# Optimization experiments

Hardware: AMD Instinct MI355X
Metric: run time of the kernel (lower is better)

## Reference

```python
import jax, jax.numpy as jnp
import numpy as np


def l2norm(x):
    return x * jax.lax.rsqrt(jnp.sum(x * x, axis=-1, keepdims=True) + 1e-12)


def vq_cosine(z, codebook, commit_w):
    # cosine-sim VQ: normalize inputs + codebook, nearest neighbor by cosine sim
    xn = l2norm(z)            # [N, D]
    en = l2norm(codebook)     # [K, D]
    sim = xn @ en.T           # [N, K]
    dist = 2.0 - 2.0 * sim    # squared euclidean between unit vectors
    idx = jnp.argmin(dist, axis=-1)           # [N]
    q = en[idx]                               # [N, D] quantized (normalized) codes
    commit = commit_w * jnp.mean((jax.lax.stop_gradient(q) - xn) ** 2)
    q_st = xn + jax.lax.stop_gradient(q - xn)  # straight-through
    return q_st, idx, commit, dist


def setup_inputs() -> dict:
    key = jax.random.key(0)
    ks = jax.random.split(key, 10)
    N, Din, H, K = 32768, 1024, 512, 1024
    s = lambda i, shp, fan: jax.random.normal(ks[i], shp, jnp.float32) * (1.0 / np.sqrt(fan))
    return {
        "h0": jax.random.normal(ks[0], (N, Din), jnp.float32),
        "W1": s(1, (Din, H), Din), "b1": jnp.zeros((H,), jnp.float32),
        "W2": s(2, (H, H), H),     "b2": jnp.zeros((H,), jnp.float32),
        "Wm": s(3, (H, H), H),     "bm": jnp.zeros((H,), jnp.float32),
        "Wt": s(4, (H, H), H),     "bt": jnp.zeros((H,), jnp.float32),
        "Wp": s(5, (H, H), H),     "bp": jnp.zeros((H,), jnp.float32),
        "cb_m": jax.random.normal(ks[6], (K, H), jnp.float32),
        "cb_t": jax.random.normal(ks[7], (K, H), jnp.float32),
        "cb_p": jax.random.normal(ks[8], (K, H), jnp.float32),
        "Wk": s(9, (H, 1), H),     "bk": jnp.zeros((1,), jnp.float32),
    }


def reference(h0, W1, b1, W2, b2, Wm, bm, Wt, bt, Wp, bp, cb_m, cb_t, cb_p, Wk, bk):
    COMMIT = 0.25
    TOP_M = 32
    # encoder: Linear-ReLU-Linear-ReLU
    H = jax.nn.relu(jax.nn.relu(h0 @ W1 + b1) @ W2 + b2)
    z_m = H @ Wm + bm
    z_t = H @ Wt + bt
    z_p = H @ Wp + bp
    q_m, k_m, cm, dist_m = vq_cosine(z_m, cb_m, COMMIT)
    q_t, k_t, ct, dist_t = vq_cosine(z_t, cb_t, COMMIT)
    q_p, k_p, cp, dist_p = vq_cosine(z_p, cb_p, COMMIT)
    codes = jnp.stack([k_m, k_t, k_p], axis=-1)           # [N, 3]
    alpha = jax.nn.sigmoid((H @ Wk + bk)[:, 0])           # [N]
    M = min(TOP_M, alpha.shape[0])
    key_idx = jax.lax.top_k(alpha, M)[1]                  # [M]
    token_emb = jnp.concatenate([q_m, q_t, q_p], axis=-1) # [N, 3*hid]
    L_vq = cm + ct + cp
    return (H, codes, key_idx, token_emb, L_vq)
```

## Files before the change

kernel.cpp:

```cpp
#include <hip/hip_runtime.h>


#define BM 128
#define BN 128
#define BK 16
#define MAXF 4096
#define MAXF1 12288
#define TAU_DIST 2e-5f
#define TAU_APPROX 1.25e-4f

#define CODES_OFF   16777216ULL
#define KEYIDX_OFF  16875520ULL
#define TOKEMB_OFF  16875552ULL
#define LVQ_OFF     67207200ULL

typedef __attribute__((ext_vector_type(8))) short short8;
typedef __attribute__((ext_vector_type(4))) float f32x4;

#define MFMA_BF16(a, b, c) __builtin_amdgcn_mfma_f32_16x16x32_bf16(a, b, c, 0, 0, 0)

__device__ __forceinline__ unsigned flip_bits(float x) {
  unsigned b = __float_as_uint(x);
  return b ^ ((unsigned)((int)b >> 31) | 0x80000000u);
}
__device__ __forceinline__ float unflip_bits(unsigned ob) {
  unsigned b = (ob & 0x80000000u) ? (ob ^ 0x80000000u) : ~ob;
  return __uint_as_float(b);
}
__device__ __forceinline__ float qdist(float dot, float rnv) {
  float sim = __fmul_rn(dot, rnv);
  return __fadd_rn(2.0f, -__fmul_rn(2.0f, sim));
}
__device__ __forceinline__ float dist_of_key(unsigned long long q) {
  return unflip_bits(~(unsigned)(q >> 32));
}
__device__ __forceinline__ void split2(float x, unsigned& h, unsigned& l) {
  unsigned b = __float_as_uint(x);
  unsigned hb = (b + 0x7FFFu + ((b >> 16) & 1u)) & 0xFFFF0000u;
  h = hb >> 16;
  float r = x - __uint_as_float(hb);
  unsigned cbits = __float_as_uint(r);
  l = (cbits + 0x7FFFu + ((cbits >> 16) & 1u)) >> 16;
}

template<int RELU>
__global__ __launch_bounds__(256)
void gemm_f32(const float* __restrict__ A, int lda,
              const float* __restrict__ B, int ldb,
              const float* __restrict__ bias,
              float* __restrict__ C, int ldc, int K)
{
  __shared__ float As[BK][BM + 4];
  __shared__ float Bs[BK][BN + 4];
  const int tid = threadIdx.x;
  const int tx = tid & 15, ty = tid >> 4;
  const long m0 = (long)blockIdx.x * BM;
  const long n0 = (long)blockIdx.y * BN;

  float acc[8][8];
#pragma unroll
  for (int i = 0; i < 8; i++)
#pragma unroll
    for (int j = 0; j < 8; j++) acc[i][j] = 0.f;

  for (int k0 = 0; k0 < K; k0 += BK) {
#pragma unroll
    for (int i = 0; i < 2; i++) {
      int f4 = tid + i * 256;
      int row = f4 >> 2, kc = (f4 & 3) * 4;
      float4 v = *(const float4*)(A + (m0 + row) * lda + k0 + kc);
      As[kc + 0][row] = v.x; As[kc + 1][row] = v.y;
      As[kc + 2][row] = v.z; As[kc + 3][row] = v.w;
    }
#pragma unroll
    for (int i = 0; i < 2; i++) {
      int f4 = tid + i * 256;
      int kr = f4 >> 5, c4 = (f4 & 31) * 4;
      *(float4*)&Bs[kr][c4] = *(const float4*)(B + (long)(k0 + kr) * ldb + n0 + c4);
    }
    __syncthreads();
#pragma unroll
    for (int kk = 0; kk < BK; kk++) {
      float a[8], b[8];
      *(float4*)&a[0] = *(const float4*)&As[kk][ty * 8];
      *(float4*)&a[4] = *(const float4*)&As[kk][ty * 8 + 4];
      *(float4*)&b[0] = *(const float4*)&Bs[kk][tx * 4];
      *(float4*)&b[4] = *(const float4*)&Bs[kk][64 + tx * 4];
#pragma unroll
      for (int i = 0; i < 8; i++)
#pragma unroll
        for (int j = 0; j < 8; j++)
          acc[i][j] = fmaf(a[i], b[j], acc[i][j]);
    }
    __syncthreads();
  }

  float bv[8];
#pragma unroll
  for (int j = 0; j < 8; j++) {
    int col = (j < 4) ? (tx * 4 + j) : (64 + tx * 4 + (j - 4));
    bv[j] = bias[n0 + col];
  }
#pragma unroll
  for (int i = 0; i < 8; i++) {
    float o[8];
#pragma unroll
    for (int j = 0; j < 8; j++) {
      float v = acc[i][j] + bv[j];
      if (RELU) v = fmaxf(v, 0.f);
      o[j] = v;
    }
    float* cp = C + (m0 + ty * 8 + i) * (long)ldc + n0;
    *(float4*)(cp + tx * 4) = *(const float4*)&o[0];
    *(float4*)(cp + 64 + tx * 4) = *(const float4*)&o[4];
  }
}

__global__ __launch_bounds__(256)
void w_split(const float* __restrict__ Wm, const float* __restrict__ Wt,
             const float* __restrict__ Wp,
             unsigned short* __restrict__ wh, unsigned short* __restrict__ wl)
{
  int t = blockIdx.x * 256 + threadIdx.x;
  int c = t >> 15, rem = t & 32767;
  int n = rem >> 6, kg = (rem & 63) * 8;
  const float* W = (c == 0) ? Wm : (c == 1) ? Wt : Wp;
  unsigned h[8], l[8];
#pragma unroll
  for (int i = 0; i < 8; i++) {
    float v = W[(size_t)(kg + i) * 512 + n];
    split2(v, h[i], l[i]);
  }
  uint4 hp, lp;
  hp.x = h[0] | (h[1] << 16); hp.y = h[2] | (h[3] << 16);
  hp.z = h[4] | (h[5] << 16); hp.w = h[6] | (h[7] << 16);
  lp.x = l[0] | (l[1] << 16); lp.y = l[2] | (l[3] << 16);
  lp.z = l[4] | (l[5] << 16); lp.w = l[6] | (l[7] << 16);
  size_t g = ((size_t)c * 512 + n) * 512 + kg;
  *(uint4*)(wh + g) = hp;
  *(uint4*)(wl + g) = lp;
}

__global__ __launch_bounds__(512, 2)
void z_mfma(const float* __restrict__ H,
            const unsigned short* __restrict__ wh,
            const unsigned short* __restrict__ wl,
            const float* __restrict__ bm, const float* __restrict__ bt,
            const float* __restrict__ bp,
            unsigned short* __restrict__ zh, unsigned short* __restrict__ zl)
{
  __shared__ unsigned short Ah[128 * 40];
  __shared__ unsigned short Al[128 * 40];
  __shared__ unsigned short Bh[512 * 40];
  __shared__ unsigned short Bl[512 * 40];

  const int tid = threadIdx.x;
  const int w = tid >> 6, wr = w >> 2, wc = w & 3;
  const int l = tid & 63, l15 = l & 15, lg = l >> 4;
  const int c = blockIdx.y;
  const long m0 = (long)blockIdx.x * BM;
  const size_t wbase = (size_t)c * 512 * 512;

  f32x4 acc[4][8];
#pragma unroll
  for (int fi = 0; fi < 4; fi++)
#pragma unroll
    for (int fj = 0; fj < 8; fj++)
#pragma unroll
      for (int r = 0; r < 4; r++) acc[fi][fj][r] = 0.f;

  for (int k0 = 0; k0 < 512; k0 += 32) {
#pragma unroll
    for (int i = 0; i < 2; i++) {
      int f4 = tid + i * 512;
      int row = f4 >> 3, kc = (f4 & 7) * 4;
      float4 v = *(const float4*)(H + (m0 + row) * 512 + k0 + kc);
      unsigned hx, lx, hy, ly, hz, lz, hw, lw;
      split2(v.x, hx, lx); split2(v.y, hy, ly);
      split2(v.z, hz, lz); split2(v.w, hw, lw);
      uint2 hp, lp;
      hp.x = hx | (hy << 16); hp.y = hz | (hw << 16);
      lp.x = lx | (ly << 16); lp.y = lz | (lw << 16);
      *(uint2*)&Ah[row * 40 + kc] = hp;
      *(uint2*)&Al[row * 40 + kc] = lp;
    }
#pragma unroll
    for (int j = 0; j < 4; j++) {
      int q = tid + j * 512;
      int n = q >> 2, kg = (q & 3) * 8;
      size_t g = wbase + (size_t)n * 512 + k0 + kg;
      *(uint4*)&Bh[n * 40 + kg] = *(const uint4*)(wh + g);
      *(uint4*)&Bl[n * 40 + kg] = *(const uint4*)(wl + g);
    }
    __syncthreads();

    short8 bh[8], bl[8];
#pragma unroll
    for (int fj = 0; fj < 8; fj++) {
      int boff = (wc * 128 + fj * 16 + l15) * 40 + lg * 8;
      bh[fj] = *(const short8*)&Bh[boff];
      bl[fj] = *(const short8*)&Bl[boff];
    }
#pragma unroll
    for (int fi = 0; fi < 4; fi++) {
      int aoff = (wr * 64 + fi * 16 + l15) * 40 + lg * 8;
      short8 ah = *(const short8*)&Ah[aoff];
      short8 al = *(const short8*)&Al[aoff];
#pragma unroll
      for (int fj = 0; fj < 8; fj++) {
        acc[fi][fj] = MFMA_BF16(ah, bh[fj], acc[fi][fj]);
        acc[fi][fj] = MFMA_BF16(al, bh[fj], acc[fi][fj]);
        acc[fi][fj] = MFMA_BF16(ah, bl[fj], acc[fi][fj]);
      }
    }
    __syncthreads();
  }

  const float* bc = (c == 0) ? bm : (c == 1) ? bt : bp;
  float bcv[8];
#pragma unroll
  for (int fj = 0; fj < 8; fj++) bcv[fj] = bc[wc * 128 + fj * 16 + l15];
#pragma unroll
  for (int fi = 0; fi < 4; fi++) {
#pragma unroll
    for (int fj = 0; fj < 8; fj++) {
      int col = wc * 128 + fj * 16 + l15;
#pragma unroll
      for (int r = 0; r < 4; r++) {
        long row = m0 + wr * 64 + fi * 16 + lg * 4 + r;
        float v = acc[fi][fj][r] + bcv[fj];
        unsigned h, lo;
        split2(v, h, lo);
        size_t g = (size_t)row * 1536 + (size_t)c * 512 + col;
        zh[g] = (unsigned short)h;
        zl[g] = (unsigned short)lo;
      }
    }
  }
}

__global__ __launch_bounds__(256)
void sim_argmax(const unsigned short* __restrict__ zh,
                const unsigned short* __restrict__ zl,
                const float* __restrict__ en,
                const unsigned short* __restrict__ en_hi,
                const unsigned short* __restrict__ en_lo,
                const float* __restrict__ rn,
                float* __restrict__ out,
                float* __restrict__ lvq,
                int* __restrict__ fc1,
                int* __restrict__ flags1)
{
  __shared__ unsigned short Ah[128 * 40];
  __shared__ unsigned short Al[128 * 40];
  __shared__ unsigned short Bh[128 * 40];
  __shared__ unsigned short Bl[128 * 40];
  __shared__ unsigned long long redk[128][2];
  __shared__ float redd[128][2];
  __shared__ int bidx[128];
  __shared__ float dsum[128];

  const int tid = threadIdx.x;
  const int w = tid >> 6, wr = w >> 1, wc = w & 1;
  const int l = tid & 63, l15 = l & 15, lg = l >> 4;
  const int c = blockIdx.y;
  const long m0 = (long)blockIdx.x * BM;
  const float* Ben = en + (size_t)c * 524288;
  const size_t cb_base = (size_t)c * 524288;

  float rrn[16];
#pragma unroll
  for (int fi = 0; fi < 4; fi++)
#pragma unroll
    for (int r = 0; r < 4; r++)
      rrn[fi * 4 + r] = rn[(long)c * 32768 + m0 + wr * 64 + fi * 16 + lg * 4 + r];

  unsigned long long best = 0ULL;
  float bestd2 = 1e30f;

  for (int ct = 0; ct < 8; ct++) {
    const int n0 = ct * 128;
    f32x4 acc[4][4];
#pragma unroll
    for (int fi = 0; fi < 4; fi++)
#pragma unroll
      for (int fj = 0; fj < 4; fj++)
#pragma unroll
        for (int r = 0; r < 4; r++) acc[fi][fj][r] = 0.f;

    for (int k0 = 0; k0 < 512; k0 += 32) {
#pragma unroll
      for (int i = 0; i < 2; i++) {
        int q = tid + i * 256;
        int row = q >> 2, kc = (q & 3) * 8;
        size_t g = (size_t)(m0 + row) * 1536 + (size_t)c * 512 + k0 + kc;
        *(uint4*)&Ah[row * 40 + kc] = *(const uint4*)(zh + g);
        *(uint4*)&Al[row * 40 + kc] = *(const uint4*)(zl + g);
      }
#pragma unroll
      for (int i = 0; i < 2; i++) {
        int q = tid + i * 256;
        int code = q >> 2, kc = (q & 3) * 8;
        size_t g = cb_base + (size_t)(n0 + code) * 512 + (k0 + kc);
        *(uint4*)&Bh[code * 40 + kc] = *(const uint4*)(en_hi + g);
        *(uint4*)&Bl[code * 40 + kc] = *(const uint4*)(en_lo + g);
      }
      __syncthreads();

      short8 bh[4], bl[4];
#pragma unroll
      for (int f = 0; f < 4; f++) {
        int boff = (wc * 64 + f * 16 + l15) * 40 + lg * 8;
        bh[f] = *(const short8*)&Bh[boff];
        bl[f] = *(const short8*)&Bl[boff];
      }
#pragma unroll
      for (int fi = 0; fi < 4; fi++) {
        int aoff = (wr * 64 + fi * 16 + l15) * 40 + lg * 8;
        short8 ah = *(const short8*)&Ah[aoff];
        short8 al = *(const short8*)&Al[aoff];
#pragma unroll
        for (int fj = 0; fj < 4; fj++) {
          acc[fi][fj] = MFMA_BF16(ah, bh[fj], acc[fi][fj]);
          acc[fi][fj] = MFMA_BF16(al, bh[fj], acc[fi][fj]);
          acc[fi][fj] = MFMA_BF16(ah, bl[fj], acc[fi][fj]);
        }
      }
      __syncthreads();
    }

#pragma unroll
    for (int fi = 0; fi < 4; fi++) {
      unsigned long long kk[4]; float dd[4];
#pragma unroll
      for (int r = 0; r < 4; r++) {
        float d1 = 1e30f, d2v = 1e30f; int bj = 0;
#pragma unroll
        for (int fj = 0; fj < 4; fj++) {
          float d = qdist(acc[fi][fj][r], rrn[fi * 4 + r]);
          if (d < d1) { d2v = d1; d1 = d; bj = fj; }
          else if (d < d2v) d2v = d;
        }
        int code = n0 + wc * 64 + bj * 16 + l15;
        kk[r] = ((unsigned long long)(~flip_bits(d1)) << 32) | (unsigned)(~code);
        dd[r] = d2v;
      }
#pragma unroll
      for (int m = 1; m < 16; m <<= 1) {
#pragma unroll
        for (int r = 0; r < 4; r++) {
          unsigned long long ok = __shfl_xor(kk[r], m, 64);
          float od = __shfl_xor(dd[r], m, 64);
          if (ok > kk[r]) { dd[r] = fminf(od, dist_of_key(kk[r])); kk[r] = ok; }
          else dd[r] = fminf(dd[r], dist_of_key(ok));
        }
      }
      if (l15 == 0) {
#pragma unroll
        for (int r = 0; r < 4; r++) {
          int row = wr * 64 + fi * 16 + lg * 4 + r;
          redk[row][wc] = kk[r];
          redd[row][wc] = dd[r];
        }
      }
    }
    __syncthreads();
    if (tid < 128) {
      unsigned long long kA = redk[tid][0]; float dA = redd[tid][0];
      unsigned long long kB = redk[tid][1]; float dB = redd[tid][1];
      unsigned long long km; float m2;
      if (kB > kA) { km = kB; m2 = fminf(dB, dist_of_key(kA)); }
      else         { km = kA; m2 = fminf(dA, dist_of_key(kB)); }
      if (km > best) {
        float oldd = (best == 0ULL) ? 1e30f : dist_of_key(best);
        bestd2 = fminf(oldd, m2);
        best = km;
      } else {
        bestd2 = fminf(bestd2, dist_of_key(km));
      }
    }
    __syncthreads();
  }

  if (tid < 128) {
    const long n = m0 + tid;
    const unsigned code = ~(unsigned)best;
    const float d1 = dist_of_key(best);
    out[CODES_OFF + (unsigned long long)n * 3 + c] = (float)code;
    bidx[tid] = (int)code;
    dsum[tid] = d1;
    if (bestd2 - d1 < TAU_APPROX) {
      int slot = atomicAdd(fc1, 1);
      if (slot < MAXF1) { flags1[2 * slot] = (int)n; flags1[2 * slot + 1] = c; }
    }
  }
  __syncthreads();
  if (tid < 64) dsum[tid] += dsum[tid + 64];
  __syncthreads();
  if (tid < 64) {
    float s = dsum[tid];
#pragma unroll
    for (int off = 32; off; off >>= 1) s += __shfl_xor(s, off);
    if (tid == 0) atomicAdd(lvq, s * (0.25f / (32768.f * 512.f)));
  }
  for (int t = tid; t < 128 * 128; t += 256) {
    int r = t >> 7, d4 = (t & 127) * 4;
    float4 v = *(const float4*)(Ben + (long)bidx[r] * 512 + d4);
    *(float4*)(out + TOKEMB_OFF + (unsigned long long)(m0 + r) * 1536 + c * 512 + d4) = v;
  }
}

__global__ __launch_bounds__(256)
void refine_fp32(const float* __restrict__ H,
                 const float* __restrict__ Wm, const float* __restrict__ bm,
                 const float* __restrict__ Wt, const float* __restrict__ bt,
                 const float* __restrict__ Wp, const float* __restrict__ bp,
                 const float* __restrict__ en,
                 const int* __restrict__ fc1, const int* __restrict__ flags1,
                 int* __restrict__ fc2, int* __restrict__ flags2,
                 float* __restrict__ out)
{
  int nf = *fc1; if (nf > MAXF1) nf = MAXF1;
  const int b = blockIdx.x;
  if (b >= nf) return;
  const int n = flags1[2 * b];
  const int c = flags1[2 * b + 1];
  const int t = threadIdx.x;

  __shared__ float sH[512];
  __shared__ float zs[512];
  __shared__ float sred[256];
  __shared__ unsigned long long wk[4];
  __shared__ float wd2[4];
  __shared__ int fcode;
  __shared__ float srn;

  const float* Wc = (c == 0) ? Wm : (c == 1) ? Wt : Wp;
  const float* bc = (c == 0) ? bm : (c == 1) ? bt : bp;

  sH[t]       = H[(size_t)n * 512 + t];
  sH[t + 256] = H[(size_t)n * 512 + 256 + t];
  __syncthreads();

  {
    float a0 = 0.f, a1 = 0.f;
    for (int i = 0; i < 512; i++) {
      float h = sH[i];
      a0 = fmaf(h, Wc[(size_t)i * 512 + t], a0);
      a1 = fmaf(h, Wc[(size_t)i * 512 + t + 256], a1);
    }
    float z0 = a0 + bc[t];
    float z1 = a1 + bc[t + 256];
    zs[t] = z0; zs[t + 256] = z1;
    sred[t] = z0 * z0 + z1 * z1;
  }
  __syncthreads();
  for (int s = 128; s > 0; s >>= 1) {
    if (t < s) sred[t] += sred[t + s];
    __syncthreads();
  }
  if (t == 0) srn = 1.f / sqrtf(sred[0] + 1e-12f);
  __syncthreads();
  const float rnv = srn;

  const int wv = t >> 6, lane = t & 63;
  float zlv[8];
#pragma unroll
  for (int m = 0; m < 8; m++) zlv[m] = zs[lane * 8 + m];

  const float* cbase = en + (size_t)c * 524288;
  unsigned long long k1 = 0ULL; float d2 = 1e30f;
  for (int j = 0; j < 256; j++) {
    int k = (j << 2) | wv;
    const float* cr = cbase + (size_t)k * 512 + lane * 8;
    float4 c0 = *(const float4*)cr, c1 = *(const float4*)(cr + 4);
    float dt = zlv[0] * c0.x + zlv[1] * c0.y + zlv[2] * c0.z + zlv[3] * c0.w
             + zlv[4] * c1.x + zlv[5] * c1.y + zlv[6] * c1.z + zlv[7] * c1.w;
#pragma unroll
    for (int off = 32; off; off >>= 1) dt += __shfl_xor(dt, off);
    float d = qdist(dt, rnv);
    unsigned long long key =
        ((unsigned long long)(~flip_bits(d)) << 32) | (unsigned)(~k);
    if (key > k1) { d2 = fminf(d2, (k1 == 0ULL) ? 1e30f : dist_of_key(k1)); k1 = key; }
    else d2 = fminf(d2, d);
  }
  if (lane == 0) { wk[wv] = k1; wd2[wv] = d2; }
  __syncthreads();
  if (t == 0) {
    unsigned long long kb = wk[0]; float s2 = wd2[0];
#pragma unroll
    for (int w = 1; w < 4; w++) {
      unsigned long long q = wk[w]; float qd2 = wd2[w];
      if (q > kb) { s2 = fminf(qd2, dist_of_key(kb)); kb = q; }
      else s2 = fminf(s2, dist_of_key(q));
    }
    int code = (int)(~(unsigned)kb);
    float d1 = dist_of_key(kb);
    out[CODES_OFF + (unsigned long long)n * 3 + c] = (float)code;
    fcode = code;
    if (s2 - d1 < TAU_DIST) {
      int slot = atomicAdd(fc2, 1);
      if (slot < MAXF) { flags2[2 * slot] = n; flags2[2 * slot + 1] = c; }
    }
  }
  __syncthreads();
  const int fk = fcode;
  if (t < 128) {
    const float* er = en + ((size_t)c * 1024 + fk) * 512;
    float4 v = ((const float4*)er)[t];
    *(float4*)(out + TOKEMB_OFF + (unsigned long long)n * 1536 + c * 512 + t * 4) = v;
  }
}

__global__ __launch_bounds__(256)
void rescue_fp64(const float* __restrict__ h0,
                 const float* __restrict__ W1, const float* __restrict__ b1,
                 const float* __restrict__ W2, const float* __restrict__ b2,
                 const float* __restrict__ Wm, const float* __restrict__ bm,
                 const float* __restrict__ Wt, const float* __restrict__ bt,
                 const float* __restrict__ Wp, const float* __restrict__ bp,
                 const float* __restrict__ cbm, const float* __restrict__ cbt,
                 const float* __restrict__ cbp,
                 const float* __restrict__ en,
                 const int* __restrict__ flag_cnt, const int* __restrict__ flags,
                 float* __restrict__ out)
{
  int nf = *flag_cnt; if (nf > MAXF) nf = MAXF;
  const int b = blockIdx.x;
  if (b >= nf) return;
  const int n = flags[2 * b];
  const int c = flags[2 * b + 1];
  const int t = threadIdx.x;

  __shared__ double s1[512];
  __shared__ double s2[512];
  __shared__ double sred[256];
  __shared__ float sd4[4];
  __shared__ int sk4[4];
  __shared__ double shz;

  const float* Wc = (c == 0) ? Wm : (c == 1) ? Wt : Wp;
  const float* bc = (c == 0) ? bm : (c == 1) ? bt : bp;
  const float* cb = (c == 0) ? cbm : (c == 1) ? cbt : cbp;
  const float* h0r = h0 + (size_t)n * 1024;

  {
    double a0 = 0.0, a1 = 0.0;
    for (int i = 0; i < 1024; i++) {
      double h = (double)h0r[i];
      a0 = fma(h, (double)W1[(size_t)i * 512 + t], a0);
      a1 = fma(h, (double)W1[(size_t)i * 512 + t + 256], a1);
    }
    s1[t]       = fmax(a0 + (double)b1[t], 0.0);
    s1[t + 256] = fmax(a1 + (double)b1[t + 256], 0.0);
  }
  __syncthreads();
  {
    double a0 = 0.0, a1 = 0.0;
    for (int i = 0; i < 512; i++) {
      double h = s1[i];
      a0 = fma(h, (double)W2[(size_t)i * 512 + t], a0);
      a1 = fma(h, (double)W2[(size_t)i * 512 + t + 256], a1);
    }
    s2[t]       = fmax(a0 + (double)b2[t], 0.0);
    s2[t + 256] = fmax(a1 + (double)b2[t + 256], 0.0);
  }
  __syncthreads();
  {
    double a0 = 0.0, a1 = 0.0;
    for (int i = 0; i < 512; i++) {
      double h = s2[i];
      a0 = fma(h, (double)Wc[(size_t)i * 512 + t], a0);
      a1 = fma(h, (double)Wc[(size_t)i * 512 + t + 256], a1);
    }
    __syncthreads();
    s1[t]       = a0 + (double)bc[t];
    s1[t + 256] = a1 + (double)bc[t + 256];
  }
  __syncthreads();
  sred[t] = s1[t] * s1[t] + s1[t + 256] * s1[t + 256];
  __syncthreads();
  for (int s = 128; s > 0; s >>= 1) {
    if (t < s) sred[t] += sred[t + s];
    __syncthreads();
  }
  if (t == 0) shz = 1.0 / sqrt(sred[0] + 1e-12);
  __syncthreads();
  const double rz = shz;

  const int wv = t >> 6, lane = t & 63;
  double zl[8];
#pragma unroll
  for (int m = 0; m < 8; m++) zl[m] = s1[lane * 8 + m];
  float bd = 1e30f; int bkk = 1 << 30;
  for (int j = 0; j < 256; j++) {
    int k = (j << 2) | wv;
    const float* cr = cb + (size_t)k * 512 + lane * 8;
    float4 c0 = *(const float4*)cr, c1 = *(const float4*)(cr + 4);
    double x0 = c0.x, x1 = c0.y, x2 = c0.z, x3 = c0.w;
    double x4 = c1.x, x5 = c1.y, x6 = c1.z, x7 = c1.w;
    double dt = zl[0]*x0 + zl[1]*x1 + zl[2]*x2 + zl[3]*x3
              + zl[4]*x4 + zl[5]*x5 + zl[6]*x6 + zl[7]*x7;
    double nc = x0*x0 + x1*x1 + x2*x2 + x3*x3 + x4*x4 + x5*x5 + x6*x6 + x7*x7;
#pragma unroll
    for (int off = 32; off; off >>= 1) {
      dt += __shfl_xor(dt, off);
      nc += __shfl_xor(nc, off);
    }
    double sim64 = dt * rz * (1.0 / sqrt(nc + 1e-12));
    float s32 = (float)sim64;
    float d32 = __fadd_rn(2.0f, -__fmul_rn(2.0f, s32));
    if (d32 < bd) { bd = d32; bkk = k; }
  }
  if (lane == 0) { sd4[wv] = bd; sk4[wv] = bkk; }
  __syncthreads();
  if (t == 0) {
    float d = sd4[0]; int k = sk4[0];
#pragma unroll
    for (int w = 1; w < 4; w++)
      if (sd4[w] < d || (sd4[w] == d && sk4[w] < k)) { d = sd4[w]; k = sk4[w]; }
    sk4[0] = k;
    out[CODES_OFF + (unsigned long long)n * 3 + c] = (float)k;
  }
  __syncthreads();
  const int fk = sk4[0];
  if (t < 128) {
    const float* er = en + ((size_t)c * 1024 + fk) * 512;
    float4 v = ((const float4*)er)[t];
    *(float4*)(out + TOKEMB_OFF + (unsigned long long)n * 1536 + c * 512 + t * 4) = v;
  }
}

__global__ __launch_bounds__(256)
void row_rnorm(const unsigned short* __restrict__ zh,
               const unsigned short* __restrict__ zl,
               float* __restrict__ rn)
{
  const int lane = threadIdx.x & 63;
  const long r = (long)blockIdx.x * 4 + (threadIdx.x >> 6);
  const int cc = (int)(r >> 15), n = (int)(r & 32767);
  const size_t base = (size_t)n * 1536 + (size_t)cc * 512 + lane * 8;
  uint4 h = *(const uint4*)(zh + base);
  uint4 lo = *(const uint4*)(zl + base);
  float s = 0.f;
  const unsigned hw[4] = {h.x, h.y, h.z, h.w};
  const unsigned lw[4] = {lo.x, lo.y, lo.z, lo.w};
#pragma unroll
  for (int i = 0; i < 4; i++) {
    float ze = __uint_as_float(hw[i] << 16) + __uint_as_float(lw[i] << 16);
    float zo = __uint_as_float(hw[i] & 0xFFFF0000u) + __uint_as_float(lw[i] & 0xFFFF0000u);
    s = fmaf(ze, ze, s);
    s = fmaf(zo, zo, s);
  }
#pragma unroll
  for (int off = 32; off; off >>= 1) s += __shfl_xor(s, off);
  if (lane == 0) rn[r] = 1.f / sqrtf(s + 1e-12f);
}

__global__ __launch_bounds__(256)
void cb_norm(const float* __restrict__ cbm, const float* __restrict__ cbt,
             const float* __restrict__ cbp, float* __restrict__ en,
             unsigned short* __restrict__ en_hi, unsigned short* __restrict__ en_lo)
{
  const int lane = threadIdx.x & 63;
  const long r = (long)blockIdx.x * 4 + (threadIdx.x >> 6);
  const int cc = (int)(r >> 10), k = (int)(r & 1023);
  const float* cb = (cc == 0) ? cbm : (cc == 1) ? cbt : cbp;
  const float* p = cb + (long)k * 512 + lane * 8;
  float4 v0 = *(const float4*)p, v1 = *(const float4*)(p + 4);
  float s = v0.x * v0.x + v0.y * v0.y + v0.z * v0.z + v0.w * v0.w
          + v1.x * v1.x + v1.y * v1.y + v1.z * v1.z + v1.w * v1.w;
#pragma unroll
  for (int off = 32; off; off >>= 1) s += __shfl_xor(s, off);
  float sc = 1.f / sqrtf(s + 1e-12f);
  v0.x *= sc; v0.y *= sc; v0.z *= sc; v0.w *= sc;
  v1.x *= sc; v1.y *= sc; v1.z *= sc; v1.w *= sc;
  const size_t g = (size_t)cc * 524288 + (size_t)k * 512 + lane * 8;
  float* q = en + g;
  *(float4*)q = v0; *(float4*)(q + 4) = v1;
  unsigned h[8], lo[8];
  split2(v0.x, h[0], lo[0]); split2(v0.y, h[1], lo[1]);
  split2(v0.z, h[2], lo[2]); split2(v0.w, h[3], lo[3]);
  split2(v1.x, h[4], lo[4]); split2(v1.y, h[5], lo[5]);
  split2(v1.z, h[6], lo[6]); split2(v1.w, h[7], lo[7]);
  uint4 hp, lp;
  hp.x = h[0] | (h[1] << 16);  hp.y = h[2] | (h[3] << 16);
  hp.z = h[4] | (h[5] << 16);  hp.w = h[6] | (h[7] << 16);
  lp.x = lo[0] | (lo[1] << 16); lp.y = lo[2] | (lo[3] << 16);
  lp.z = lo[4] | (lo[5] << 16); lp.w = lo[6] | (lo[7] << 16);
  *(uint4*)(en_hi + g) = hp;
  *(uint4*)(en_lo + g) = lp;
}

__global__ __launch_bounds__(256)
void logits_alpha(const float* __restrict__ H, const float* __restrict__ Wk,
                  const float* __restrict__ bk, float* __restrict__ alpha)
{
  const int lane = threadIdx.x & 63;
  const long n = (long)blockIdx.x * 4 + (threadIdx.x >> 6);
  const float* p = H + n * 512 + lane * 8;
  const float* w = Wk + lane * 8;
  float4 a0 = *(const float4*)p, a1 = *(const float4*)(p + 4);
  float4 w0 = *(const float4*)w, w1 = *(const float4*)(w + 4);
  float s = a0.x * w0.x + a0.y * w0.y + a0.z * w0.z + a0.w * w0.w
          + a1.x * w1.x + a1.y * w1.y + a1.z * w1.z + a1.w * w1.w;
#pragma unroll
  for (int off = 32; off; off >>= 1) s += __shfl_xor(s, off);
  if (lane == 0) alpha[n] = 1.f / (1.f + expf(-(s + bk[0])));
}

__global__ __launch_bounds__(1024)
void topk32(const float* __restrict__ alpha, float* __restrict__ out)
{
  __shared__ unsigned long long sk[1024];
  const int tid = threadIdx.x;
  unsigned long long prev = ~0ULL;
  for (int it = 0; it < 32; it++) {
    unsigned long long best = 0;
#pragma unroll 4
    for (int i = tid; i < 32768; i += 1024) {
      unsigned long long key =
          ((unsigned long long)flip_bits(alpha[i]) << 32) | (unsigned)(~i);
      if (key < prev && key > best) best = key;
    }
    sk[tid] = best;
    __syncthreads();
    for (int s = 512; s > 0; s >>= 1) {
      if (tid < s) { unsigned long long q = sk[tid + s]; if (q > sk[tid]) sk[tid] = q; }
      __syncthreads();
    }
    unsigned long long sel = sk[0];
    __syncthreads();
    if (tid == 0) out[it] = (float)(~(unsigned)sel);
    prev = sel;
  }
}

extern "C" void kernel_launch(void* const* d_in, const int* in_sizes, int n_in,
                              void* d_out, int out_size, void* d_ws, size_t ws_size,
                              hipStream_t stream)
{
  (void)in_sizes; (void)n_in; (void)out_size; (void)ws_size;
  const float* h0  = (const float*)d_in[0];
  const float* W1  = (const float*)d_in[1];
  const float* b1  = (const float*)d_in[2];
  const float* W2  = (const float*)d_in[3];
  const float* b2  = (const float*)d_in[4];
  const float* Wm  = (const float*)d_in[5];
  const float* bm  = (const float*)d_in[6];
  const float* Wt  = (const float*)d_in[7];
  const float* bt  = (const float*)d_in[8];
  const float* Wp  = (const float*)d_in[9];
  const float* bp  = (const float*)d_in[10];
  const float* cbm = (const float*)d_in[11];
  const float* cbt = (const float*)d_in[12];
  const float* cbp = (const float*)d_in[13];
  const float* Wk  = (const float*)d_in[14];
  const float* bk  = (const float*)d_in[15];
  float* out = (float*)d_out;
  float* ws  = (float*)d_ws;

  float* h1 = ws;
  unsigned short* zh = (unsigned short*)ws;
  unsigned short* zl = (unsigned short*)ws + 50331648ULL;
  float* en = ws + 50331648ULL;
  float* rn = ws + 51904512ULL;
  float* al = ws + 52002816ULL;
  int* fc1    = (int*)(ws + 52035584ULL);
  int* flags1 = (int*)(ws + 52035585ULL);
  int* fc2    = (int*)(ws + 52060161ULL);
  int* flags2 = (int*)(ws + 52060162ULL);
  unsigned short* en_hi = (unsigned short*)(ws + 52068356ULL);
  unsigned short* en_lo = (unsigned short*)(ws + 52854788ULL);
  unsigned short* Wh = (unsigned short*)(ws + 53641220ULL);
  unsigned short* Wl = (unsigned short*)(ws + 54034436ULL);
  float* H  = out;
  float* lvq = out + LVQ_OFF;

  hipMemsetAsync(lvq, 0, sizeof(float), stream);
  hipMemsetAsync(fc1, 0, sizeof(int), stream);
  hipMemsetAsync(fc2, 0, sizeof(int), stream);

  gemm_f32<1><<<dim3(256, 4), 256, 0, stream>>>(h0, 1024, W1, 512, b1, h1, 512, 1024);
  gemm_f32<1><<<dim3(256, 4), 256, 0, stream>>>(h1, 512,  W2, 512, b2, H,  512, 512);

  w_split<<<384, 256, 0, stream>>>(Wm, Wt, Wp, Wh, Wl);
  z_mfma<<<dim3(256, 3), 512, 0, stream>>>(H, Wh, Wl, bm, bt, bp, zh, zl);

  row_rnorm<<<24576, 256, 0, stream>>>(zh, zl, rn);
  cb_norm<<<768, 256, 0, stream>>>(cbm, cbt, cbp, en, en_hi, en_lo);
  sim_argmax<<<dim3(256, 3), 256, 0, stream>>>(zh, zl, en, en_hi, en_lo, rn, out, lvq,
                                               fc1, flags1);
  refine_fp32<<<MAXF1, 256, 0, stream>>>(H, Wm, bm, Wt, bt, Wp, bp, en,
                                         fc1, flags1, fc2, flags2, out);
  rescue_fp64<<<MAXF, 256, 0, stream>>>(h0, W1, b1, W2, b2, Wm, bm, Wt, bt, Wp, bp,
                                        cbm, cbt, cbp, en, fc2, flags2, out);
  logits_alpha<<<8192, 256, 0, stream>>>(H, Wk, bk, al);
  topk32<<<1, 1024, 0, stream>>>(al, out + KEYIDX_OFF);
}
```

Before: 2.494 ms.

## Move encoder GEMMs to split-bf16 MFMA and stage z epilogue through LDS

Replaces the scalar FP32 GEMMs for the two encoder layers with a generalized MFMA kernel. It uses a three-product bf16 hi/lo split to approximate FP32 accuracy, with weights pre-split by a generic split kernel. The z projection epilogue now stages hi/lo planes in shared memory and writes coalesced 16-byte vectors instead of scattered 2-byte stores. The costs are three extra MFMAs per tile and some precision loss versus true FP32, which the refine/rescue passes must absorb. The three z projections also become separate launches, and the workspace layout is reshuffled.

```diff
diff --git a/kernel.cpp b/kernel.cpp
--- a/kernel.cpp
+++ b/kernel.cpp
@@ -2,8 +2,6 @@
 
 
 #define BM 128
-#define BN 128
-#define BK 16
 #define MAXF 4096
 #define MAXF1 12288
 #define TAU_DIST 2e-5f
@@ -43,88 +41,14 @@
   l = (cbits + 0x7FFFu + ((cbits >> 16) & 1u)) >> 16;
 }
 
-template<int RELU>
 __global__ __launch_bounds__(256)
-void gemm_f32(const float* __restrict__ A, int lda,
-              const float* __restrict__ B, int ldb,
-              const float* __restrict__ bias,
-              float* __restrict__ C, int ldc, int K)
-{
-  __shared__ float As[BK][BM + 4];
-  __shared__ float Bs[BK][BN + 4];
-  const int tid = threadIdx.x;
-  const int tx = tid & 15, ty = tid >> 4;
-  const long m0 = (long)blockIdx.x * BM;
-  const long n0 = (long)blockIdx.y * BN;
-
-  float acc[8][8];
-#pragma unroll
-  for (int i = 0; i < 8; i++)
-#pragma unroll
-    for (int j = 0; j < 8; j++) acc[i][j] = 0.f;
-
-  for (int k0 = 0; k0 < K; k0 += BK) {
-#pragma unroll
-    for (int i = 0; i < 2; i++) {
-      int f4 = tid + i * 256;
-      int row = f4 >> 2, kc = (f4 & 3) * 4;
-      float4 v = *(const float4*)(A + (m0 + row) * lda + k0 + kc);
-      As[kc + 0][row] = v.x; As[kc + 1][row] = v.y;
-      As[kc + 2][row] = v.z; As[kc + 3][row] = v.w;
-    }
-#pragma unroll
-    for (int i = 0; i < 2; i++) {
-      int f4 = tid + i * 256;
-      int kr = f4 >> 5, c4 = (f4 & 31) * 4;
-      *(float4*)&Bs[kr][c4] = *(const float4*)(B + (long)(k0 + kr) * ldb + n0 + c4);
-    }
-    __syncthreads();
-#pragma unroll
-    for (int kk = 0; kk < BK; kk++) {
-      float a[8], b[8];
-      *(float4*)&a[0] = *(const float4*)&As[kk][ty * 8];
-      *(float4*)&a[4] = *(const float4*)&As[kk][ty * 8 + 4];
-      *(float4*)&b[0] = *(const float4*)&Bs[kk][tx * 4];
-      *(float4*)&b[4] = *(const float4*)&Bs[kk][64 + tx * 4];
-#pragma unroll
-      for (int i = 0; i < 8; i++)
-#pragma unroll
-        for (int j = 0; j < 8; j++)
-          acc[i][j] = fmaf(a[i], b[j], acc[i][j]);
-    }
-    __syncthreads();
-  }
-
-  float bv[8];
-#pragma unroll
-  for (int j = 0; j < 8; j++) {
-    int col = (j < 4) ? (tx * 4 + j) : (64 + tx * 4 + (j - 4));
-    bv[j] = bias[n0 + col];
-  }
-#pragma unroll
-  for (int i = 0; i < 8; i++) {
-    float o[8];
-#pragma unroll
-    for (int j = 0; j < 8; j++) {
-      float v = acc[i][j] + bv[j];
-      if (RELU) v = fmaxf(v, 0.f);
-      o[j] = v;
-    }
-    float* cp = C + (m0 + ty * 8 + i) * (long)ldc + n0;
-    *(float4*)(cp + tx * 4) = *(const float4*)&o[0];
-    *(float4*)(cp + 64 + tx * 4) = *(const float4*)&o[4];
-  }
-}
-
-__global__ __launch_bounds__(256)
-void w_split(const float* __restrict__ Wm, const float* __restrict__ Wt,
-             const float* __restrict__ Wp,
-             unsigned short* __restrict__ wh, unsigned short* __restrict__ wl)
+void wsplit_g(const float* __restrict__ W,
+              unsigned short* __restrict__ wh, unsigned short* __restrict__ wl,
+              int K)
 {
   int t = blockIdx.x * 256 + threadIdx.x;
-  int c = t >> 15, rem = t & 32767;
-  int n = rem >> 6, kg = (rem & 63) * 8;
-  const float* W = (c == 0) ? Wm : (c == 1) ? Wt : Wp;
+  int kg8 = K >> 3;
+  int n = t / kg8, kg = (t % kg8) * 8;
   unsigned h[8], l[8];
 #pragma unroll
   for (int i = 0; i < 8; i++) {
@@ -136,30 +60,31 @@
   hp.z = h[4] | (h[5] << 16); hp.w = h[6] | (h[7] << 16);
   lp.x = l[0] | (l[1] << 16); lp.y = l[2] | (l[3] << 16);
   lp.z = l[4] | (l[5] << 16); lp.w = l[6] | (l[7] << 16);
-  size_t g = ((size_t)c * 512 + n) * 512 + kg;
+  size_t g = (size_t)n * K + kg;
   *(uint4*)(wh + g) = hp;
   *(uint4*)(wl + g) = lp;
 }
 
+template<int RELU, int OUTPLANES>
 __global__ __launch_bounds__(512, 2)
-void z_mfma(const float* __restrict__ H,
-            const unsigned short* __restrict__ wh,
-            const unsigned short* __restrict__ wl,
-            const float* __restrict__ bm, const float* __restrict__ bt,
-            const float* __restrict__ bp,
-            unsigned short* __restrict__ zh, unsigned short* __restrict__ zl)
-{
-  __shared__ unsigned short Ah[128 * 40];
-  __shared__ unsigned short Al[128 * 40];
-  __shared__ unsigned short Bh[512 * 40];
-  __shared__ unsigned short Bl[512 * 40];
+void mfma_gemm(const float* __restrict__ A, int lda, int K,
+               const unsigned short* __restrict__ wh,
+               const unsigned short* __restrict__ wl,
+               const float* __restrict__ bias,
+               float* __restrict__ Cf, int ldc,
+               unsigned short* __restrict__ zh, unsigned short* __restrict__ zl,
+               int ldz, int colOff)
+{
+  __shared__ __align__(16) unsigned char smem[102400];
+  unsigned short* Ah = (unsigned short*)smem;
+  unsigned short* Al = Ah + 5120;
+  unsigned short* Bh = Al + 5120;
+  unsigned short* Bl = Bh + 20480;
 
   const int tid = threadIdx.x;
   const int w = tid >> 6, wr = w >> 2, wc = w & 3;
   const int l = tid & 63, l15 = l & 15, lg = l >> 4;
-  const int c = blockIdx.y;
   const long m0 = (long)blockIdx.x * BM;
-  const size_t wbase = (size_t)c * 512 * 512;
 
   f32x4 acc[4][8];
 #pragma unroll
@@ -169,12 +94,12 @@
 #pragma unroll
       for (int r = 0; r < 4; r++) acc[fi][fj][r] = 0.f;
 
-  for (int k0 = 0; k0 < 512; k0 += 32) {
+  for (int k0 = 0; k0 < K; k0 += 32) {
 #pragma unroll
     for (int i = 0; i < 2; i++) {
       int f4 = tid + i * 512;
       int row = f4 >> 3, kc = (f4 & 7) * 4;
-      float4 v = *(const float4*)(H + (m0 + row) * 512 + k0 + kc);
+      float4 v = *(const float4*)(A + (m0 + row) * lda + k0 + kc);
       unsigned hx, lx, hy, ly, hz, lz, hw, lw;
       split2(v.x, hx, lx); split2(v.y, hy, ly);
       split2(v.z, hz, lz); split2(v.w, hw, lw);
@@ -188,7 +113,7 @@
     for (int j = 0; j < 4; j++) {
       int q = tid + j * 512;
       int n = q >> 2, kg = (q & 3) * 8;
-      size_t g = wbase + (size_t)n * 512 + k0 + kg;
+      size_t g = (size_t)n * K + k0 + kg;
       *(uint4*)&Bh[n * 40 + kg] = *(const uint4*)(wh + g);
       *(uint4*)&Bl[n * 40 + kg] = *(const uint4*)(wl + g);
     }
@@ -216,24 +141,54 @@
     __syncthreads();
   }
 
-  const float* bc = (c == 0) ? bm : (c == 1) ? bt : bp;
   float bcv[8];
 #pragma unroll
-  for (int fj = 0; fj < 8; fj++) bcv[fj] = bc[wc * 128 + fj * 16 + l15];
-#pragma unroll
-  for (int fi = 0; fi < 4; fi++) {
-#pragma unroll
-    for (int fj = 0; fj < 8; fj++) {
-      int col = wc * 128 + fj * 16 + l15;
-#pragma unroll
-      for (int r = 0; r < 4; r++) {
-        long row = m0 + wr * 64 + fi * 16 + lg * 4 + r;
-        float v = acc[fi][fj][r] + bcv[fj];
-        unsigned h, lo;
-        split2(v, h, lo);
-        size_t g = (size_t)row * 1536 + (size_t)c * 512 + col;
-        zh[g] = (unsigned short)h;
-        zl[g] = (unsigned short)lo;
+  for (int fj = 0; fj < 8; fj++) bcv[fj] = bias[wc * 128 + fj * 16 + l15];
+
+  if (OUTPLANES == 0) {
+#pragma unroll
+    for (int fi = 0; fi < 4; fi++)
+#pragma unroll
+      for (int fj = 0; fj < 8; fj++) {
+        int col = wc * 128 + fj * 16 + l15;
+#pragma unroll
+        for (int r = 0; r < 4; r++) {
+          long row = m0 + wr * 64 + fi * 16 + lg * 4 + r;
+          float v = acc[fi][fj][r] + bcv[fj];
+          if (RELU) v = fmaxf(v, 0.f);
+          Cf[row * (long)ldc + col] = v;
+        }
+      }
+  } else {
+    unsigned short* ep = (unsigned short*)smem;
+#pragma unroll
+    for (int half = 0; half < 2; half++) {
+#pragma unroll
+      for (int pl = 0; pl < 2; pl++) {
+        if (wr == half) {
+#pragma unroll
+          for (int fi = 0; fi < 4; fi++)
+#pragma unroll
+            for (int fj = 0; fj < 8; fj++) {
+              int col = wc * 128 + fj * 16 + l15;
+#pragma unroll
+              for (int r = 0; r < 4; r++) {
+                int row = fi * 16 + lg * 4 + r;
+                float v = acc[fi][fj][r] + bcv[fj];
+                unsigned h, lo;
+                split2(v, h, lo);
+                ep[row * 512 + col] = (unsigned short)(pl ? lo : h);
+              }
+            }
+        }
+        __syncthreads();
+        unsigned short* dst = pl ? zl : zh;
+        for (int u = tid; u < 4096; u += 512) {
+          int row = u >> 6, c8 = (u & 63) * 8;
+          size_t g = (size_t)(m0 + half * 64 + row) * ldz + colOff + c8;
+          *(uint4*)(dst + g) = *(const uint4*)(ep + row * 512 + c8);
+        }
+        __syncthreads();
       }
     }
   }
@@ -760,9 +715,13 @@
   float* out = (float*)d_out;
   float* ws  = (float*)d_ws;
 
-  float* h1 = ws;
   unsigned short* zh = (unsigned short*)ws;
   unsigned short* zl = (unsigned short*)ws + 50331648ULL;
+  float* h1 = ws;
+  unsigned short* W1h = (unsigned short*)ws + 33554432ULL;
+  unsigned short* W1l = W1h + 524288ULL;
+  unsigned short* W2h = W1l + 524288ULL;
+  unsigned short* W2l = W2h + 262144ULL;
   float* en = ws + 50331648ULL;
   float* rn = ws + 51904512ULL;
   float* al = ws + 52002816ULL;
@@ -781,11 +740,26 @@
   hipMemsetAsync(fc1, 0, sizeof(int), stream);
   hipMemsetAsync(fc2, 0, sizeof(int), stream);
 
-  gemm_f32<1><<<dim3(256, 4), 256, 0, stream>>>(h0, 1024, W1, 512, b1, h1, 512, 1024);
-  gemm_f32<1><<<dim3(256, 4), 256, 0, stream>>>(h1, 512,  W2, 512, b2, H,  512, 512);
-
-  w_split<<<384, 256, 0, stream>>>(Wm, Wt, Wp, Wh, Wl);
-  z_mfma<<<dim3(256, 3), 512, 0, stream>>>(H, Wh, Wl, bm, bt, bp, zh, zl);
+  wsplit_g<<<256, 256, 0, stream>>>(W1, W1h, W1l, 1024);
+  wsplit_g<<<128, 256, 0, stream>>>(W2, W2h, W2l, 512);
+  wsplit_g<<<128, 256, 0, stream>>>(Wm, Wh + 0 * 262144, Wl + 0 * 262144, 512);
+  wsplit_g<<<128, 256, 0, stream>>>(Wt, Wh + 1 * 262144, Wl + 1 * 262144, 512);
+  wsplit_g<<<128, 256, 0, stream>>>(Wp, Wh + 2 * 262144, Wl + 2 * 262144, 512);
+
+  mfma_gemm<1, 0><<<256, 512, 0, stream>>>(h0, 1024, 1024, W1h, W1l, b1,
+                                           h1, 512, nullptr, nullptr, 0, 0);
+  mfma_gemm<1, 0><<<256, 512, 0, stream>>>(h1, 512, 512, W2h, W2l, b2,
+                                           H, 512, nullptr, nullptr, 0, 0);
+
+  mfma_gemm<0, 1><<<256, 512, 0, stream>>>(H, 512, 512, Wh + 0 * 262144,
+                                           Wl + 0 * 262144, bm, nullptr, 0,
+                                           zh, zl, 1536, 0);
+  mfma_gemm<0, 1><<<256, 512, 0, stream>>>(H, 512, 512, Wh + 1 * 262144,
+                                           Wl + 1 * 262144, bt, nullptr, 0,
+                                           zh, zl, 1536, 512);
+  mfma_gemm<0, 1><<<256, 512, 0, stream>>>(H, 512, 512, Wh + 2 * 262144,
+                                           Wl + 2 * 262144, bp, nullptr, 0,
+                                           zh, zl, 1536, 1024);
 
   row_rnorm<<<24576, 256, 0, stream>>>(zh, zl, rn);
   cb_norm<<<768, 256, 0, stream>>>(cbm, cbt, cbp, en, en_hi, en_lo);
```

Measured after the change: 2.304 ms. -7.6%, faster.
